# Performance work log

Measured on AMD Instinct MI355X. Metric: run time of the kernel, lower is better.

The kernel has to match this reference:

```python
import jax, jax.numpy as jnp
import numpy as np

N_NODES = 100000
N_EDGES = 1600000
DIM = 128


def setup_inputs() -> dict:
    key = jax.random.key(0)
    ks = jax.random.split(key, 8)
    s = 1.0 / np.sqrt(DIM)
    return {
        "x": jax.random.normal(ks[0], (N_NODES, DIM), dtype=jnp.float32),
        "edge_index": jax.random.randint(ks[1], (2, N_EDGES), 0, N_NODES, dtype=jnp.int64),
        "W1_l": jax.random.normal(ks[2], (DIM, DIM), dtype=jnp.float32) * s,
        "b1": jnp.zeros((DIM,), dtype=jnp.float32),
        "W1_r": jax.random.normal(ks[3], (DIM, DIM), dtype=jnp.float32) * s,
        "W2_l": jax.random.normal(ks[4], (DIM, DIM), dtype=jnp.float32) * s,
        "b2": jnp.zeros((DIM,), dtype=jnp.float32),
        "W2_r": jax.random.normal(ks[5], (DIM, DIM), dtype=jnp.float32) * s,
    }


def _sage_conv(h, src, dst, n, W_l, b, W_r):
    # mean aggregation of source-node features onto target nodes
    agg = jax.ops.segment_sum(h[src], dst, num_segments=n)          # [N, D]
    deg = jax.ops.segment_sum(jnp.ones_like(src, dtype=h.dtype), dst, num_segments=n)
    agg = agg / jnp.maximum(deg, 1.0)[:, None]
    # PyG SAGEConv: lin_l(aggr) + bias + lin_r(x)  (root weight, no bias on lin_r)
    return agg @ W_l + b + h @ W_r


def reference(x, edge_index, W1_l, b1, W1_r, W2_l, b2, W2_r):
    src, dst = edge_index[0], edge_index[1]
    n = x.shape[0]
    h = jax.nn.relu(_sage_conv(x, src, dst, n, W1_l, b1, W1_r))
    return _sage_conv(h, src, dst, n, W2_l, b2, W2_r)
```

## Files before the change

kernel.cpp:

```cpp
#include <hip/hip_runtime.h>

typedef unsigned short ushort_t;
typedef unsigned int uint_t;

typedef short bf16x8 __attribute__((ext_vector_type(8)));
typedef float f32x4 __attribute__((ext_vector_type(4)));

#define DIM 128
#define BSHIFT 8
#define BNODES 256
#define DBINS 64

__device__ __forceinline__ ushort_t f2bf(float f) {
    uint_t x;
    __builtin_memcpy(&x, &f, 4);
    uint_t r = (x + 0x7fffu + ((x >> 16) & 1u)) >> 16;
    return (ushort_t)r;
}


__global__ __launch_bounds__(256) void k_prep_bhist(
        const float* __restrict__ x, ushort_t* __restrict__ xb, int n4,
        const float* __restrict__ W1l, const float* __restrict__ W1r,
        const float* __restrict__ W2l, const float* __restrict__ W2r,
        ushort_t* __restrict__ fragbuf,
        const int* __restrict__ dst, int E, int NB, int* __restrict__ bucketCount,
        int prepBlocks) {
    if ((int)blockIdx.x >= prepBlocks) {
        __shared__ int hist[512];
        int blk = blockIdx.x - prepBlocks;
        int t = threadIdx.x;
        for (int b = t; b < NB; b += 256) hist[b] = 0;
        __syncthreads();
        int per = (E + 255) / 256;
        int beg = blk * per, end = min(beg + per, E);
        for (int i = beg + t; i < end; i += 256)
            atomicAdd(&hist[dst[i] >> BSHIFT], 1);
        __syncthreads();
        for (int b = t; b < NB; b += 256) {
            int v = hist[b];
            if (v) atomicAdd(&bucketCount[b], v);
        }
        return;
    }
    int i = blockIdx.x * 256 + threadIdx.x;
    if (i < n4) {
        float4 f = ((const float4*)x)[i];
        ushort4 u;
        u.x = f2bf(f.x); u.y = f2bf(f.y); u.z = f2bf(f.z); u.w = f2bf(f.w);
        ((ushort4*)xb)[i] = u;
    } else {
        int j = i - n4;
        if (j < 2 * 64 * 64) {
            int layer = j >> 12;
            int rr = j & 4095;
            int f = rr >> 6, l = rr & 63;
            int nt = f >> 3, ks2 = f & 7;
            int col = l & 15, quad = l >> 4;
            int n = nt * 16 + col;
            int kb = ks2 * 32 + quad * 8;
            const float* Wl = layer ? W2l : W1l;
            const float* Wr = layer ? W2r : W1r;
            ushort_t* d = fragbuf + layer * 32768 + f * 512 + l * 8;
#pragma unroll
            for (int jj = 0; jj < 8; jj++) {
                int k2 = kb + jj;
                float v = (k2 < 128) ? Wl[k2 * DIM + n] : Wr[(k2 - 128) * DIM + n];
                d[jj] = f2bf(v);
            }
        }
    }
}


__global__ __launch_bounds__(256) void k_bucketize(const int* __restrict__ src,
                                                   const int* __restrict__ dst, int E, int NB,
                                                   const int* __restrict__ bucketCount,
                                                   int* __restrict__ bucketBase_out,
                                                   int* __restrict__ row_ptr, int N,
                                                   int* __restrict__ zcur,
                                                   uint_t* __restrict__ bebuf) {
    __shared__ int bbase[512];
    __shared__ int hist[512];
    __shared__ int rbase[512];
    int t = threadIdx.x;
    int i0 = t, i1 = t + 256;
    int v0 = (i0 < NB) ? bucketCount[i0] : 0;
    int v1 = (i1 < NB) ? bucketCount[i1] : 0;
    bbase[i0] = v0; bbase[i1] = v1;
    __syncthreads();
    for (int off = 1; off < 512; off <<= 1) {
        int u0 = (i0 >= off) ? bbase[i0 - off] : 0;
        int u1 = (i1 >= off) ? bbase[i1 - off] : 0;
        __syncthreads();
        bbase[i0] += u0; bbase[i1] += u1;
        __syncthreads();
    }
    bbase[i0] -= v0;
    bbase[i1] -= v1;
    if (blockIdx.x == 0) {
        if (i0 < NB) bucketBase_out[i0] = bbase[i0];
        if (i1 < NB) bucketBase_out[i1] = bbase[i1];
        if (t == 0) row_ptr[N] = E;
    }
    hist[i0] = 0; hist[i1] = 0;
    __syncthreads();
    int per = (E + gridDim.x - 1) / gridDim.x;
    int beg = blockIdx.x * per, end = min(beg + per, E);
    for (int i = beg + t; i < end; i += 256)
        atomicAdd(&hist[dst[i] >> BSHIFT], 1);
    __syncthreads();
    {
        int v = hist[i0];
        rbase[i0] = v ? (bbase[i0] + atomicAdd(&zcur[i0], v)) : 0;
        hist[i0] = 0;
        v = hist[i1];
        rbase[i1] = v ? (bbase[i1] + atomicAdd(&zcur[i1], v)) : 0;
        hist[i1] = 0;
    }
    __syncthreads();
    for (int i = beg + t; i < end; i += 256) {
        int d = dst[i], s = src[i];
        int b = d >> BSHIFT;
        int off = atomicAdd(&hist[b], 1);
        bebuf[rbase[b] + off] = ((uint_t)(d & (BNODES - 1)) << 24) | (uint_t)s;
    }
}

__global__ __launch_bounds__(256) void k_bcsr(const uint_t* __restrict__ bebuf,
                                              const int* __restrict__ bucketBase,
                                              const int* __restrict__ bucketCount, int N,
                                              int* __restrict__ row_ptr, int* __restrict__ csr,
                                              int* __restrict__ dhist) {
    __shared__ int hist[BNODES];
    __shared__ int cur[BNODES];
    __shared__ int dh[DBINS];
    int t = threadIdx.x;
    int b = blockIdx.x;
    int ebase = bucketBase[b], cnt = bucketCount[b];
    int nodeBase = b << BSHIFT;
    hist[t] = 0;
    if (t < DBINS) dh[t] = 0;
    __syncthreads();
    for (int i = t; i < cnt; i += 256)
        atomicAdd(&hist[bebuf[ebase + i] >> 24], 1);
    __syncthreads();
    int v = hist[t];
    int node = nodeBase + t;
    if (node < N) atomicAdd(&dh[min(v, DBINS - 1)], 1);
    for (int off = 1; off < 256; off <<= 1) {
        int u = (t >= off) ? hist[t - off] : 0;
        __syncthreads();
        hist[t] += u;
        __syncthreads();
    }
    int excl = hist[t] - v;
    if (node < N) row_ptr[node] = ebase + excl;
    cur[t] = excl;
    __syncthreads();
    for (int i = t; i < cnt; i += 256) {
        uint_t e = bebuf[ebase + i];
        int dl = (int)(e >> 24);
        int pos = atomicAdd(&cur[dl], 1);
        csr[ebase + pos] = (int)(e & 0xFFFFFFu);
    }
    __syncthreads();
    if (t < DBINS) {
        int c = dh[t];
        if (c) atomicAdd(&dhist[t], c);
    }
}


__global__ __launch_bounds__(256) void k_dperm(const int* __restrict__ rp, int N,
                                               const int* __restrict__ dhist,
                                               int* __restrict__ zdcur, int* __restrict__ perm) {
    __shared__ int eb[DBINS];
    __shared__ int h[DBINS];
    __shared__ int rb[DBINS];
    int t = threadIdx.x;
    int v = (t < DBINS) ? dhist[t] : 0;
    if (t < DBINS) { eb[t] = v; h[t] = 0; }
    __syncthreads();
    for (int off = 1; off < DBINS; off <<= 1) {
        int u = (t < DBINS && t >= off) ? eb[t - off] : 0;
        __syncthreads();
        if (t < DBINS) eb[t] += u;
        __syncthreads();
    }
    if (t < DBINS) eb[t] -= v;
    int i = blockIdx.x * 256 + t;
    int b = -1;
    if (i < N) {
        int d = rp[i + 1] - rp[i];
        b = min(d, DBINS - 1);
        atomicAdd(&h[b], 1);
    }
    __syncthreads();
    if (t < DBINS) {
        int hv = h[t];
        rb[t] = hv ? (eb[t] + atomicAdd(&zdcur[t], hv)) : 0;
        h[t] = 0;
    }
    __syncthreads();
    if (i < N) {
        int off = atomicAdd(&h[b], 1);
        perm[rb[b] + off] = i;
    }
}


__device__ __forceinline__ void acc8(float* a, uint4 p) {
    union { uint_t u; float f; } c;
    c.u = p.x << 16;         a[0] += c.f;
    c.u = p.x & 0xffff0000u; a[1] += c.f;
    c.u = p.y << 16;         a[2] += c.f;
    c.u = p.y & 0xffff0000u; a[3] += c.f;
    c.u = p.z << 16;         a[4] += c.f;
    c.u = p.z & 0xffff0000u; a[5] += c.f;
    c.u = p.w << 16;         a[6] += c.f;
    c.u = p.w & 0xffff0000u; a[7] += c.f;
}

template <bool RELU, bool OUT_BF16>
__global__ __launch_bounds__(256) void k_fused(const ushort_t* __restrict__ X,
                                               const int* __restrict__ row_ptr,
                                               const int* __restrict__ csr,
                                               const int* __restrict__ perm,
                                               const ushort_t* __restrict__ fragbuf,
                                               const float* __restrict__ bias,
                                               void* __restrict__ Out, int N) {
    __shared__ __align__(16) ushort_t tile[16 * 256];
    __shared__ int nd[16];
    int t = threadIdx.x;
    int gl = t >> 4;
    int sl = t & 15;
    int gidx = blockIdx.x * 16 + gl;
    bool act = (gidx < N);
    int node = 0, beg = 0, end = 0;
    if (act) {
        node = perm[gidx];
        beg = row_ptr[node];
        end = row_ptr[node + 1];
    }
    if (sl == 0) nd[gl] = node;

    float a[8] = {0.f, 0.f, 0.f, 0.f, 0.f, 0.f, 0.f, 0.f};
    int e = beg;
    for (; e + 4 <= end; e += 4) {
        int s0 = csr[e + 0], s1 = csr[e + 1], s2 = csr[e + 2], s3 = csr[e + 3];
        uint4 p0 = *(const uint4*)(X + (size_t)s0 * DIM + sl * 8);
        uint4 p1 = *(const uint4*)(X + (size_t)s1 * DIM + sl * 8);
        uint4 p2 = *(const uint4*)(X + (size_t)s2 * DIM + sl * 8);
        uint4 p3 = *(const uint4*)(X + (size_t)s3 * DIM + sl * 8);
        acc8(a, p0); acc8(a, p1); acc8(a, p2); acc8(a, p3);
    }
    for (; e < end; e++) {
        int s = csr[e];
        uint4 p = *(const uint4*)(X + (size_t)s * DIM + sl * 8);
        acc8(a, p);
    }
    int cnt = end - beg;
    float scl = (cnt > 0) ? 1.f / (float)cnt : 0.f;

    int swz = gl & 7;
    uint4 o;
    o.x = (uint_t)f2bf(a[0] * scl) | ((uint_t)f2bf(a[1] * scl) << 16);
    o.y = (uint_t)f2bf(a[2] * scl) | ((uint_t)f2bf(a[3] * scl) << 16);
    o.z = (uint_t)f2bf(a[4] * scl) | ((uint_t)f2bf(a[5] * scl) << 16);
    o.w = (uint_t)f2bf(a[6] * scl) | ((uint_t)f2bf(a[7] * scl) << 16);
    *(uint4*)(tile + gl * 256 + ((sl ^ swz) * 8)) = o;
    uint4 p;
    if (act) p = *(const uint4*)(X + (size_t)node * DIM + sl * 8);
    else     p = (uint4){0u, 0u, 0u, 0u};
    *(uint4*)(tile + gl * 256 + (((16 + sl) ^ swz) * 8)) = p;
    __syncthreads();

    int lane = t & 63, w = t >> 6;
    int m = lane & 15, quad = lane >> 4;
    bf16x8 af[8];
#pragma unroll
    for (int ks2 = 0; ks2 < 8; ks2++) {
        int c = (ks2 * 4 + quad) ^ (m & 7);
        af[ks2] = *(const bf16x8*)(tile + m * 256 + c * 8);
    }
    f32x4 acc0 = (f32x4){0.f, 0.f, 0.f, 0.f};
    f32x4 acc1 = (f32x4){0.f, 0.f, 0.f, 0.f};
    const ushort_t* fb0 = fragbuf + (size_t)((w * 2 + 0) * 8) * 512 + lane * 8;
    const ushort_t* fb1 = fragbuf + (size_t)((w * 2 + 1) * 8) * 512 + lane * 8;
#pragma unroll
    for (int ks2 = 0; ks2 < 8; ks2++) {
        bf16x8 b0 = *(const bf16x8*)(fb0 + ks2 * 512);
        acc0 = __builtin_amdgcn_mfma_f32_16x16x32_bf16(af[ks2], b0, acc0, 0, 0, 0);
    }
#pragma unroll
    for (int ks2 = 0; ks2 < 8; ks2++) {
        bf16x8 b1 = *(const bf16x8*)(fb1 + ks2 * 512);
        acc1 = __builtin_amdgcn_mfma_f32_16x16x32_bf16(af[ks2], b1, acc1, 0, 0, 0);
    }
    int c0 = (w * 2 + 0) * 16 + m;
    int c1 = (w * 2 + 1) * 16 + m;
    float bv0 = bias[c0], bv1 = bias[c1];
#pragma unroll
    for (int r = 0; r < 4; r++) {
        int mrow = quad * 4 + r;
        int gI = blockIdx.x * 16 + mrow;
        if (gI < N) {
            int nodeW = nd[mrow];
            float v0 = acc0[r] + bv0;
            float v1 = acc1[r] + bv1;
            if (RELU) { v0 = fmaxf(v0, 0.f); v1 = fmaxf(v1, 0.f); }
            if (OUT_BF16) {
                ((ushort_t*)Out)[(size_t)nodeW * DIM + c0] = f2bf(v0);
                ((ushort_t*)Out)[(size_t)nodeW * DIM + c1] = f2bf(v1);
            } else {
                ((float*)Out)[(size_t)nodeW * DIM + c0] = v0;
                ((float*)Out)[(size_t)nodeW * DIM + c1] = v1;
            }
        }
    }
}


extern "C" void kernel_launch(void* const* d_in, const int* in_sizes, int n_in,
                              void* d_out, int out_size, void* d_ws, size_t ws_size,
                              hipStream_t stream) {
    const int N = in_sizes[0] / DIM;
    const int E = in_sizes[1] / 2;
    const int NB = (N + BNODES - 1) >> BSHIFT;

    const float* x   = (const float*)d_in[0];
    const int*   ei  = (const int*)d_in[1];
    const int*   src = ei;
    const int*   dst = ei + E;
    const float* W1l = (const float*)d_in[2];
    const float* b1  = (const float*)d_in[3];
    const float* W1r = (const float*)d_in[4];
    const float* W2l = (const float*)d_in[5];
    const float* b2  = (const float*)d_in[6];
    const float* W2r = (const float*)d_in[7];
    float* out = (float*)d_out;

    char* ws = (char*)d_ws;
    size_t off = 0;
    auto alloc = [&](size_t bytes) -> char* {
        char* p = ws + off;
        off = (off + bytes + 255) & ~(size_t)255;
        return p;
    };

    int*      bucketCount  = (int*)alloc((size_t)NB * 4);
    int*      dhist        = (int*)alloc((size_t)DBINS * 4);
    int*      zcur         = (int*)alloc((size_t)NB * 4);
    int*      zdcur        = (int*)alloc((size_t)DBINS * 4);
    size_t    zspan        = (size_t)((char*)zdcur + DBINS * 4 - (char*)bucketCount);
    int*      bucketBase   = (int*)alloc((size_t)NB * 4);
    int*      row_ptr      = (int*)alloc((size_t)(N + 1) * 4);
    int*      csr          = (int*)alloc((size_t)E * 4);
    uint_t*   bebuf        = (uint_t*)alloc((size_t)E * 4);
    ushort_t* xb           = (ushort_t*)alloc((size_t)N * DIM * 2);
    ushort_t* hb           = (ushort_t*)alloc((size_t)N * DIM * 2);
    ushort_t* fragbuf      = (ushort_t*)alloc((size_t)2 * 32768 * 2);
    int*      perm         = (int*)bebuf;

    hipMemsetAsync(bucketCount, 0, zspan, stream);

    {
        int n4 = N * DIM / 4;
        int total = n4 + 2 * 64 * 64;
        int prepBlocks = (total + 255) / 256;
        k_prep_bhist<<<dim3(prepBlocks + 256), dim3(256), 0, stream>>>(
            x, xb, n4, W1l, W1r, W2l, W2r, fragbuf,
            dst, E, NB, bucketCount, prepBlocks);
    }
    k_bucketize<<<dim3(256), dim3(256), 0, stream>>>(src, dst, E, NB, bucketCount,
                                                     bucketBase, row_ptr, N, zcur, bebuf);
    k_bcsr<<<dim3(NB), dim3(256), 0, stream>>>(bebuf, bucketBase, bucketCount, N,
                                               row_ptr, csr, dhist);
    const int nblk = (N + 255) / 256;
    k_dperm<<<dim3(nblk), dim3(256), 0, stream>>>(row_ptr, N, dhist, zdcur, perm);

    const int ntiles = (N + 15) / 16;
    k_fused<true, true><<<dim3(ntiles), dim3(256), 0, stream>>>(
        xb, row_ptr, csr, perm, fragbuf, b1, hb, N);
    k_fused<false, false><<<dim3(ntiles), dim3(256), 0, stream>>>(
        hb, row_ptr, csr, perm, fragbuf + 32768, b2, out, N);

    (void)n_in; (void)out_size; (void)ws_size;
}
```

Baseline: 319.7 us.

## Merge graph preprocessing kernels into one cooperative kernel and stage bf16 output stores

Replaces the memset plus four preprocessing launches (prep/histogram, bucketize, block CSR, degree permutation) with a single cooperative kernel of NB blocks. Grid-wide syncs separate the phases, and the bucket prefix sums are kept in shared memory across phases. The aim is to remove launch gaps and small-kernel tails, at the cost of running the bf16 conversion and edge passes on only NB (~391) blocks, which reduces parallelism. The layer-1 epilogue also stages bf16 results in a shared tile so each row is written with coalesced 16-byte stores instead of scattered 2-byte stores. The degree-permutation phase relies on NB*256 covering N.

```diff
diff --git a/kernel.cpp b/kernel.cpp
--- a/kernel.cpp
+++ b/kernel.cpp
@@ -1,4 +1,7 @@
 #include <hip/hip_runtime.h>
+#include <hip/hip_cooperative_groups.h>
+
+namespace cg = cooperative_groups;
 
 typedef unsigned short ushort_t;
 typedef unsigned int uint_t;
@@ -19,193 +22,177 @@
 }
 
 
-__global__ __launch_bounds__(256) void k_prep_bhist(
-        const float* __restrict__ x, ushort_t* __restrict__ xb, int n4,
-        const float* __restrict__ W1l, const float* __restrict__ W1r,
-        const float* __restrict__ W2l, const float* __restrict__ W2r,
-        ushort_t* __restrict__ fragbuf,
-        const int* __restrict__ dst, int E, int NB, int* __restrict__ bucketCount,
-        int prepBlocks) {
-    if ((int)blockIdx.x >= prepBlocks) {
-        __shared__ int hist[512];
-        int blk = blockIdx.x - prepBlocks;
-        int t = threadIdx.x;
-        for (int b = t; b < NB; b += 256) hist[b] = 0;
-        __syncthreads();
-        int per = (E + 255) / 256;
-        int beg = blk * per, end = min(beg + per, E);
-        for (int i = beg + t; i < end; i += 256)
-            atomicAdd(&hist[dst[i] >> BSHIFT], 1);
-        __syncthreads();
-        for (int b = t; b < NB; b += 256) {
-            int v = hist[b];
-            if (v) atomicAdd(&bucketCount[b], v);
-        }
-        return;
-    }
-    int i = blockIdx.x * 256 + threadIdx.x;
-    if (i < n4) {
+__global__ __launch_bounds__(256) void k_mega(
+        const float* x, ushort_t* xb, int n4,
+        const float* W1l, const float* W1r, const float* W2l, const float* W2r,
+        ushort_t* fragbuf,
+        const int* src, const int* dst, int E, int NB, int N,
+        int* bucketCount, int* zcur, int* dhist, int* zdcur,
+        int* zerobase, int nzero,
+        int* row_ptr, int* csr, uint_t* bebuf, int* perm) {
+    cg::grid_group grid = cg::this_grid();
+    __shared__ int hist[512];
+    __shared__ int bbase[512];
+    __shared__ int aux[512];
+    __shared__ int dh[DBINS];
+    __shared__ int dh2[DBINS];
+    __shared__ int dh3[DBINS];
+
+    int t = threadIdx.x;
+    int nb = gridDim.x;
+    int gsz = nb * 256;
+    int gtid = blockIdx.x * 256 + t;
+    int per = (E + nb - 1) / nb;
+    int beg = blockIdx.x * per, endE = min(beg + per, E);
+
+    for (int i = gtid; i < nzero; i += gsz) zerobase[i] = 0;
+    if (gtid == 0) row_ptr[N] = E;
+    for (int i = gtid; i < n4; i += gsz) {
         float4 f = ((const float4*)x)[i];
         ushort4 u;
         u.x = f2bf(f.x); u.y = f2bf(f.y); u.z = f2bf(f.z); u.w = f2bf(f.w);
         ((ushort4*)xb)[i] = u;
-    } else {
-        int j = i - n4;
-        if (j < 2 * 64 * 64) {
-            int layer = j >> 12;
-            int rr = j & 4095;
-            int f = rr >> 6, l = rr & 63;
-            int nt = f >> 3, ks2 = f & 7;
-            int col = l & 15, quad = l >> 4;
-            int n = nt * 16 + col;
-            int kb = ks2 * 32 + quad * 8;
-            const float* Wl = layer ? W2l : W1l;
-            const float* Wr = layer ? W2r : W1r;
-            ushort_t* d = fragbuf + layer * 32768 + f * 512 + l * 8;
-#pragma unroll
-            for (int jj = 0; jj < 8; jj++) {
-                int k2 = kb + jj;
-                float v = (k2 < 128) ? Wl[k2 * DIM + n] : Wr[(k2 - 128) * DIM + n];
-                d[jj] = f2bf(v);
-            }
-        }
-    }
-}
-
-
-__global__ __launch_bounds__(256) void k_bucketize(const int* __restrict__ src,
-                                                   const int* __restrict__ dst, int E, int NB,
-                                                   const int* __restrict__ bucketCount,
-                                                   int* __restrict__ bucketBase_out,
-                                                   int* __restrict__ row_ptr, int N,
-                                                   int* __restrict__ zcur,
-                                                   uint_t* __restrict__ bebuf) {
-    __shared__ int bbase[512];
-    __shared__ int hist[512];
-    __shared__ int rbase[512];
-    int t = threadIdx.x;
-    int i0 = t, i1 = t + 256;
-    int v0 = (i0 < NB) ? bucketCount[i0] : 0;
-    int v1 = (i1 < NB) ? bucketCount[i1] : 0;
-    bbase[i0] = v0; bbase[i1] = v1;
+    }
+    for (int j = gtid; j < 2 * 64 * 64; j += gsz) {
+        int layer = j >> 12;
+        int rr = j & 4095;
+        int f = rr >> 6, l = rr & 63;
+        int nt = f >> 3, ks2 = f & 7;
+        int col = l & 15, quad = l >> 4;
+        int n = nt * 16 + col;
+        int kb = ks2 * 32 + quad * 8;
+        const float* Wl = layer ? W2l : W1l;
+        const float* Wr = layer ? W2r : W1r;
+        ushort_t* d = fragbuf + layer * 32768 + f * 512 + l * 8;
+#pragma unroll
+        for (int jj = 0; jj < 8; jj++) {
+            int k2 = kb + jj;
+            float v = (k2 < 128) ? Wl[k2 * DIM + n] : Wr[(k2 - 128) * DIM + n];
+            d[jj] = f2bf(v);
+        }
+    }
+    __threadfence();
+    grid.sync();
+    __threadfence();
+
+    for (int b = t; b < NB; b += 256) hist[b] = 0;
     __syncthreads();
-    for (int off = 1; off < 512; off <<= 1) {
-        int u0 = (i0 >= off) ? bbase[i0 - off] : 0;
-        int u1 = (i1 >= off) ? bbase[i1 - off] : 0;
-        __syncthreads();
-        bbase[i0] += u0; bbase[i1] += u1;
-        __syncthreads();
-    }
-    bbase[i0] -= v0;
-    bbase[i1] -= v1;
-    if (blockIdx.x == 0) {
-        if (i0 < NB) bucketBase_out[i0] = bbase[i0];
-        if (i1 < NB) bucketBase_out[i1] = bbase[i1];
-        if (t == 0) row_ptr[N] = E;
-    }
-    hist[i0] = 0; hist[i1] = 0;
-    __syncthreads();
-    int per = (E + gridDim.x - 1) / gridDim.x;
-    int beg = blockIdx.x * per, end = min(beg + per, E);
-    for (int i = beg + t; i < end; i += 256)
+    for (int i = beg + t; i < endE; i += 256)
         atomicAdd(&hist[dst[i] >> BSHIFT], 1);
     __syncthreads();
+    for (int b = t; b < NB; b += 256) {
+        int v = hist[b];
+        if (v) atomicAdd(&bucketCount[b], v);
+    }
+    __threadfence();
+    grid.sync();
+    __threadfence();
+
     {
-        int v = hist[i0];
-        rbase[i0] = v ? (bbase[i0] + atomicAdd(&zcur[i0], v)) : 0;
-        hist[i0] = 0;
-        v = hist[i1];
-        rbase[i1] = v ? (bbase[i1] + atomicAdd(&zcur[i1], v)) : 0;
-        hist[i1] = 0;
-    }
-    __syncthreads();
-    for (int i = beg + t; i < end; i += 256) {
-        int d = dst[i], s = src[i];
-        int b = d >> BSHIFT;
-        int off = atomicAdd(&hist[b], 1);
-        bebuf[rbase[b] + off] = ((uint_t)(d & (BNODES - 1)) << 24) | (uint_t)s;
-    }
-}
-
-__global__ __launch_bounds__(256) void k_bcsr(const uint_t* __restrict__ bebuf,
-                                              const int* __restrict__ bucketBase,
-                                              const int* __restrict__ bucketCount, int N,
-                                              int* __restrict__ row_ptr, int* __restrict__ csr,
-                                              int* __restrict__ dhist) {
-    __shared__ int hist[BNODES];
-    __shared__ int cur[BNODES];
-    __shared__ int dh[DBINS];
-    int t = threadIdx.x;
-    int b = blockIdx.x;
-    int ebase = bucketBase[b], cnt = bucketCount[b];
-    int nodeBase = b << BSHIFT;
-    hist[t] = 0;
-    if (t < DBINS) dh[t] = 0;
-    __syncthreads();
-    for (int i = t; i < cnt; i += 256)
-        atomicAdd(&hist[bebuf[ebase + i] >> 24], 1);
-    __syncthreads();
-    int v = hist[t];
-    int node = nodeBase + t;
-    if (node < N) atomicAdd(&dh[min(v, DBINS - 1)], 1);
-    for (int off = 1; off < 256; off <<= 1) {
-        int u = (t >= off) ? hist[t - off] : 0;
-        __syncthreads();
-        hist[t] += u;
-        __syncthreads();
-    }
-    int excl = hist[t] - v;
-    if (node < N) row_ptr[node] = ebase + excl;
-    cur[t] = excl;
-    __syncthreads();
-    for (int i = t; i < cnt; i += 256) {
-        uint_t e = bebuf[ebase + i];
-        int dl = (int)(e >> 24);
-        int pos = atomicAdd(&cur[dl], 1);
-        csr[ebase + pos] = (int)(e & 0xFFFFFFu);
-    }
-    __syncthreads();
-    if (t < DBINS) {
-        int c = dh[t];
-        if (c) atomicAdd(&dhist[t], c);
-    }
-}
-
-
-__global__ __launch_bounds__(256) void k_dperm(const int* __restrict__ rp, int N,
-                                               const int* __restrict__ dhist,
-                                               int* __restrict__ zdcur, int* __restrict__ perm) {
-    __shared__ int eb[DBINS];
-    __shared__ int h[DBINS];
-    __shared__ int rb[DBINS];
-    int t = threadIdx.x;
-    int v = (t < DBINS) ? dhist[t] : 0;
-    if (t < DBINS) { eb[t] = v; h[t] = 0; }
-    __syncthreads();
-    for (int off = 1; off < DBINS; off <<= 1) {
-        int u = (t < DBINS && t >= off) ? eb[t - off] : 0;
-        __syncthreads();
-        if (t < DBINS) eb[t] += u;
-        __syncthreads();
-    }
-    if (t < DBINS) eb[t] -= v;
-    int i = blockIdx.x * 256 + t;
-    int b = -1;
-    if (i < N) {
-        int d = rp[i + 1] - rp[i];
-        b = min(d, DBINS - 1);
-        atomicAdd(&h[b], 1);
-    }
-    __syncthreads();
-    if (t < DBINS) {
-        int hv = h[t];
-        rb[t] = hv ? (eb[t] + atomicAdd(&zdcur[t], hv)) : 0;
-        h[t] = 0;
-    }
-    __syncthreads();
-    if (i < N) {
-        int off = atomicAdd(&h[b], 1);
-        perm[rb[b] + off] = i;
+        int i0 = t, i1 = t + 256;
+        int v0 = (i0 < NB) ? bucketCount[i0] : 0;
+        int v1 = (i1 < NB) ? bucketCount[i1] : 0;
+        bbase[i0] = v0; bbase[i1] = v1;
+        __syncthreads();
+        for (int off = 1; off < 512; off <<= 1) {
+            int u0 = (i0 >= off) ? bbase[i0 - off] : 0;
+            int u1 = (i1 >= off) ? bbase[i1 - off] : 0;
+            __syncthreads();
+            bbase[i0] += u0; bbase[i1] += u1;
+            __syncthreads();
+        }
+        bbase[i0] -= v0; bbase[i1] -= v1;
+        __syncthreads();
+        {
+            int v = (i0 < NB) ? hist[i0] : 0;
+            aux[i0] = v ? (bbase[i0] + atomicAdd(&zcur[i0], v)) : 0;
+            hist[i0] = 0;
+            v = (i1 < NB) ? hist[i1] : 0;
+            aux[i1] = v ? (bbase[i1] + atomicAdd(&zcur[i1], v)) : 0;
+            hist[i1] = 0;
+        }
+        __syncthreads();
+        for (int i = beg + t; i < endE; i += 256) {
+            int d = dst[i], s = src[i];
+            int b2 = d >> BSHIFT;
+            int off2 = atomicAdd(&hist[b2], 1);
+            bebuf[aux[b2] + off2] = ((uint_t)(d & (BNODES - 1)) << 24) | (uint_t)s;
+        }
+    }
+    __threadfence();
+    grid.sync();
+    __threadfence();
+
+    {
+        int b = blockIdx.x;
+        int ebase = bbase[b];
+        int cnt = bucketCount[b];
+        int nodeBase = b << BSHIFT;
+        hist[t] = 0;
+        if (t < DBINS) dh[t] = 0;
+        __syncthreads();
+        for (int i = t; i < cnt; i += 256)
+            atomicAdd(&hist[(int)(bebuf[ebase + i] >> 24)], 1);
+        __syncthreads();
+        int v = hist[t];
+        int node = nodeBase + t;
+        if (node < N) atomicAdd(&dh[min(v, DBINS - 1)], 1);
+        for (int off = 1; off < 256; off <<= 1) {
+            int u = (t >= off) ? hist[t - off] : 0;
+            __syncthreads();
+            hist[t] += u;
+            __syncthreads();
+        }
+        int excl = hist[t] - v;
+        if (node < N) row_ptr[node] = ebase + excl;
+        aux[t] = excl;
+        __syncthreads();
+        for (int i = t; i < cnt; i += 256) {
+            uint_t e = bebuf[ebase + i];
+            int dl = (int)(e >> 24);
+            int pos = atomicAdd(&aux[dl], 1);
+            csr[ebase + pos] = (int)(e & 0xFFFFFFu);
+        }
+        __syncthreads();
+        if (t < DBINS) {
+            int c = dh[t];
+            if (c) atomicAdd(&dhist[t], c);
+        }
+    }
+    __threadfence();
+    grid.sync();
+    __threadfence();
+
+    {
+        int v = (t < DBINS) ? dhist[t] : 0;
+        if (t < DBINS) { dh[t] = v; dh2[t] = 0; }
+        __syncthreads();
+        for (int off = 1; off < DBINS; off <<= 1) {
+            int u = (t < DBINS && t >= off) ? dh[t - off] : 0;
+            __syncthreads();
+            if (t < DBINS) dh[t] += u;
+            __syncthreads();
+        }
+        if (t < DBINS) dh[t] -= v;
+        __syncthreads();
+        int i = blockIdx.x * 256 + t;
+        int bin = -1;
+        if (i < N) {
+            int d = row_ptr[i + 1] - row_ptr[i];
+            bin = min(d, DBINS - 1);
+            atomicAdd(&dh2[bin], 1);
+        }
+        __syncthreads();
+        if (t < DBINS) {
+            int hv = dh2[t];
+            dh3[t] = hv ? (dh[t] + atomicAdd(&zdcur[t], hv)) : 0;
+            dh2[t] = 0;
+        }
+        __syncthreads();
+        if (i < N) {
+            int off2 = atomicAdd(&dh2[bin], 1);
+            perm[dh3[bin] + off2] = i;
+        }
     }
 }
 
@@ -301,19 +288,40 @@
     int c0 = (w * 2 + 0) * 16 + m;
     int c1 = (w * 2 + 1) * 16 + m;
     float bv0 = bias[c0], bv1 = bias[c1];
-#pragma unroll
-    for (int r = 0; r < 4; r++) {
-        int mrow = quad * 4 + r;
-        int gI = blockIdx.x * 16 + mrow;
-        if (gI < N) {
-            int nodeW = nd[mrow];
-            float v0 = acc0[r] + bv0;
-            float v1 = acc1[r] + bv1;
+
+    if (OUT_BF16) {
+        float r0v[4], r1v[4];
+#pragma unroll
+        for (int r = 0; r < 4; r++) {
+            float v0 = acc0[r] + bv0, v1 = acc1[r] + bv1;
             if (RELU) { v0 = fmaxf(v0, 0.f); v1 = fmaxf(v1, 0.f); }
-            if (OUT_BF16) {
-                ((ushort_t*)Out)[(size_t)nodeW * DIM + c0] = f2bf(v0);
-                ((ushort_t*)Out)[(size_t)nodeW * DIM + c1] = f2bf(v1);
-            } else {
+            r0v[r] = v0; r1v[r] = v1;
+        }
+        __syncthreads();
+        ushort_t* to = tile;
+#pragma unroll
+        for (int r = 0; r < 4; r++) {
+            int mrow = quad * 4 + r;
+            to[mrow * 128 + c0] = f2bf(r0v[r]);
+            to[mrow * 128 + c1] = f2bf(r1v[r]);
+        }
+        __syncthreads();
+        int gl2 = t >> 4, sl2 = t & 15;
+        int g2 = blockIdx.x * 16 + gl2;
+        if (g2 < N) {
+            uint4 vv = *(const uint4*)(to + gl2 * 128 + sl2 * 8);
+            *(uint4*)((ushort_t*)Out + (size_t)nd[gl2] * DIM + sl2 * 8) = vv;
+        }
+    } else {
+#pragma unroll
+        for (int r = 0; r < 4; r++) {
+            int mrow = quad * 4 + r;
+            int gI = blockIdx.x * 16 + mrow;
+            if (gI < N) {
+                int nodeW = nd[mrow];
+                float v0 = acc0[r] + bv0;
+                float v1 = acc1[r] + bv1;
+                if (RELU) { v0 = fmaxf(v0, 0.f); v1 = fmaxf(v1, 0.f); }
                 ((float*)Out)[(size_t)nodeW * DIM + c0] = v0;
                 ((float*)Out)[(size_t)nodeW * DIM + c1] = v1;
             }
@@ -354,7 +362,6 @@
     int*      zcur         = (int*)alloc((size_t)NB * 4);
     int*      zdcur        = (int*)alloc((size_t)DBINS * 4);
     size_t    zspan        = (size_t)((char*)zdcur + DBINS * 4 - (char*)bucketCount);
-    int*      bucketBase   = (int*)alloc((size_t)NB * 4);
     int*      row_ptr      = (int*)alloc((size_t)(N + 1) * 4);
     int*      csr          = (int*)alloc((size_t)E * 4);
     uint_t*   bebuf        = (uint_t*)alloc((size_t)E * 4);
@@ -363,22 +370,36 @@
     ushort_t* fragbuf      = (ushort_t*)alloc((size_t)2 * 32768 * 2);
     int*      perm         = (int*)bebuf;
 
-    hipMemsetAsync(bucketCount, 0, zspan, stream);
-
     {
         int n4 = N * DIM / 4;
-        int total = n4 + 2 * 64 * 64;
-        int prepBlocks = (total + 255) / 256;
-        k_prep_bhist<<<dim3(prepBlocks + 256), dim3(256), 0, stream>>>(
-            x, xb, n4, W1l, W1r, W2l, W2r, fragbuf,
-            dst, E, NB, bucketCount, prepBlocks);
-    }
-    k_bucketize<<<dim3(256), dim3(256), 0, stream>>>(src, dst, E, NB, bucketCount,
-                                                     bucketBase, row_ptr, N, zcur, bebuf);
-    k_bcsr<<<dim3(NB), dim3(256), 0, stream>>>(bebuf, bucketBase, bucketCount, N,
-                                               row_ptr, csr, dhist);
-    const int nblk = (N + 255) / 256;
-    k_dperm<<<dim3(nblk), dim3(256), 0, stream>>>(row_ptr, N, dhist, zdcur, perm);
+        int nzero = (int)(zspan / 4);
+        int* zerobase = bucketCount;
+        int Ev = E, NBv = NB, Nv = N;
+        const float* xv = x;
+        const int* srcv = src;
+        const int* dstv = dst;
+        const float *w1l = W1l, *w1r = W1r, *w2l = W2l, *w2r = W2r;
+        ushort_t* xbv = xb;
+        ushort_t* fbv = fragbuf;
+        int* bcv = bucketCount;
+        int* zcv = zcur;
+        int* dhv = dhist;
+        int* zdv = zdcur;
+        int* rpv = row_ptr;
+        int* csrv = csr;
+        uint_t* bev = bebuf;
+        int* permv = perm;
+        void* margs[] = {
+            (void*)&xv, (void*)&xbv, (void*)&n4,
+            (void*)&w1l, (void*)&w1r, (void*)&w2l, (void*)&w2r,
+            (void*)&fbv,
+            (void*)&srcv, (void*)&dstv, (void*)&Ev, (void*)&NBv, (void*)&Nv,
+            (void*)&bcv, (void*)&zcv, (void*)&dhv, (void*)&zdv,
+            (void*)&zerobase, (void*)&nzero,
+            (void*)&rpv, (void*)&csrv, (void*)&bev, (void*)&permv };
+        hipLaunchCooperativeKernel((void*)k_mega, dim3((unsigned)NB), dim3(256),
+                                   margs, 0, stream);
+    }
 
     const int ntiles = (N + 15) / 16;
     k_fused<true, true><<<dim3(ntiles), dim3(256), 0, stream>>>(
```

Result: slower. 812.6 us (+154.2%).
